# Kernel tuning notes

Measured on AMD Instinct MI355X. Metric: run time of the kernel, lower is better.

The kernel has to match this reference:

```python
import math
import jax, jax.numpy as jnp
import numpy as np

B, S, IN_DIM = 8, 1024, 3
D, H, FF, L, OUT = 512, 8, 2048, 4, 6
DH = D // H


def layernorm(x, g, b, eps=1e-5):
    mu = jnp.mean(x, axis=-1, keepdims=True)
    var = jnp.mean((x - mu) ** 2, axis=-1, keepdims=True)
    return (x - mu) * jax.lax.rsqrt(var + eps) * g + b


def positional_encoding(seq_len, d):
    pos = jnp.arange(seq_len, dtype=jnp.float32)[:, None]
    div = jnp.exp(jnp.arange(0, d, 2, dtype=jnp.float32) * (-math.log(10000.0) / d))
    pe = jnp.zeros((seq_len, d), dtype=jnp.float32)
    pe = pe.at[:, 0::2].set(jnp.sin(pos * div))
    pe = pe.at[:, 1::2].set(jnp.cos(pos * div))
    return pe  # [S, D]


def setup_inputs() -> dict:
    key = jax.random.key(0)
    ks = jax.random.split(key, 16)
    s = 0.02
    inp = {
        'x': jax.random.normal(ks[0], (B, S, IN_DIM), dtype=jnp.float32),
        'Wproj': jax.random.normal(ks[1], (IN_DIM, D), dtype=jnp.float32) * s,
        'bproj': jnp.zeros((D,), jnp.float32),
        'gp': jnp.ones((D,), jnp.float32), 'bp': jnp.zeros((D,), jnp.float32),
        'Wq': jax.random.normal(ks[2], (L, D, D), dtype=jnp.float32) * s,
        'Wk': jax.random.normal(ks[3], (L, D, D), dtype=jnp.float32) * s,
        'Wv': jax.random.normal(ks[4], (L, D, D), dtype=jnp.float32) * s,
        'Wo': jax.random.normal(ks[5], (L, D, D), dtype=jnp.float32) * s,
        'g1': jnp.ones((L, D), jnp.float32), 'b1': jnp.zeros((L, D), jnp.float32),
        'W1': jax.random.normal(ks[6], (L, D, FF), dtype=jnp.float32) * s,
        'W2': jax.random.normal(ks[7], (L, FF, D), dtype=jnp.float32) * s,
        'g2': jnp.ones((L, D), jnp.float32), 'b2': jnp.zeros((L, D), jnp.float32),
        'gf': jnp.ones((D,), jnp.float32), 'bf': jnp.zeros((D,), jnp.float32),
        'Wout': jax.random.normal(ks[8], (D, OUT), dtype=jnp.float32) * s,
        'bout': jnp.zeros((OUT,), jnp.float32),
    }
    return inp


def reference(x, Wproj, bproj, gp, bp, Wq, Wk, Wv, Wo, g1, b1,
              W1, W2, g2, b2, gf, bf, Wout, bout):
    # padding mask: True where all features are zero
    mask = jnp.sum(jnp.abs(x), axis=-1) == 0  # [B, S]
    h = x @ Wproj + bproj                     # [B, S, D]
    h = h + positional_encoding(h.shape[1], D)[None]
    h = layernorm(h, gp, bp)
    scale = 1.0 / math.sqrt(DH)
    for l in range(L):
        q = (h @ Wq[l]).reshape(B, S, H, DH)
        k = (h @ Wk[l]).reshape(B, S, H, DH)
        v = (h @ Wv[l]).reshape(B, S, H, DH)
        scores = jnp.einsum('bqhd,bkhd->bhqk', q, k) * scale  # [B,H,S,S]
        scores = jnp.where(mask[:, None, None, :], -jnp.inf, scores)
        attn = jax.nn.softmax(scores, axis=-1)
        o = jnp.einsum('bhqk,bkhd->bqhd', attn, v).reshape(B, S, D) @ Wo[l]
        h = layernorm(h + o, g1[l], b1[l])
        ff = jax.nn.silu(h @ W1[l]) @ W2[l]
        h = layernorm(h + ff, g2[l], b2[l])
    h = layernorm(h, gf, bf)
    not_pad = (~mask).astype(h.dtype)                      # [B, S]
    pooled = jnp.sum(h * not_pad[..., None], axis=1) / (
        jnp.sum(not_pad, axis=1, keepdims=True) + 1e-8)    # [B, D]
    return pooled @ Wout + bout                            # [B, OUT]
```

## Files before the change

### kernel.cpp

```cpp
#include <hip/hip_runtime.h>
#include <math.h>
#include <stdint.h>

namespace {

constexpr int Bc = 8, Sc = 1024, Dc = 512, Hc = 8, FFc = 2048, Lc = 4, OUTc = 6;
constexpr int QS = 1536;

typedef __attribute__((ext_vector_type(8))) short  bf16x8;
typedef __attribute__((ext_vector_type(4))) float  f32x4;

__device__ __forceinline__ void ld4(float d[4], const float* s) {
    float4 t = *(const float4*)s;
    d[0] = t.x; d[1] = t.y; d[2] = t.z; d[3] = t.w;
}
__device__ __forceinline__ float bf2f(unsigned short u) {
    union { uint32_t i; float f; } c; c.i = ((uint32_t)u) << 16; return c.f;
}
__device__ __forceinline__ unsigned short f2bf(float f) {
    union { float f; uint32_t i; } c; c.f = f;
    uint32_t r = c.i + 0x7FFF + ((c.i >> 16) & 1);
    return (unsigned short)(r >> 16);
}

#define GLDS16(gp, lp) __builtin_amdgcn_global_load_lds(                      \
    (const __attribute__((address_space(1))) uint32_t*)(gp),                  \
    (__attribute__((address_space(3))) uint32_t*)(lp), 16, 0, 0)

__global__ __launch_bounds__(256) void castT(
    const float* __restrict__ in, unsigned short* __restrict__ out,
    int K, int N, size_t in_ls, size_t out_ls)
{
    __shared__ float t[64][65];
    const int k0 = blockIdx.x << 6, n0 = blockIdx.y << 6;
    in  += (size_t)blockIdx.z * in_ls;
    out += (size_t)blockIdx.z * out_ls;
    const int c = threadIdx.x & 63, r4 = threadIdx.x >> 6;
    #pragma unroll
    for (int it = 0; it < 16; ++it) {
        const int r = (it << 2) + r4;
        t[r][c] = in[(size_t)(k0 + r) * N + n0 + c];
    }
    __syncthreads();
    #pragma unroll
    for (int it = 0; it < 16; ++it) {
        const int r = (it << 2) + r4;
        out[(size_t)(n0 + r) * K + k0 + c] = f2bf(t[c][r]);
    }
}

__global__ __launch_bounds__(256) void proj_pe_ln(
    const float* __restrict__ x, const float* __restrict__ Wproj,
    const float* __restrict__ bproj, const float* __restrict__ gp,
    const float* __restrict__ bp, float* __restrict__ h,
    unsigned short* __restrict__ hbf, float* __restrict__ notpad,
    float* __restrict__ maskadd)
{
    const int wave = threadIdx.x >> 6, lane = threadIdx.x & 63;
    const int tok = (blockIdx.x << 2) + wave;
    const int s = tok & (Sc - 1);
    const float x0 = x[tok * 3 + 0], x1 = x[tok * 3 + 1], x2 = x[tok * 3 + 2];
    if (lane == 0) {
        const bool pad = (fabsf(x0) + fabsf(x1) + fabsf(x2) == 0.0f);
        notpad[tok]  = pad ? 0.0f : 1.0f;
        maskadd[tok] = pad ? -1e30f : 0.0f;
    }
    const float c = -logf(10000.0f) / (float)Dc;
    float v[8];
    float sum = 0.f, sumsq = 0.f;
    #pragma unroll
    for (int g = 0; g < 2; ++g) {
        const int dbase = (g << 8) + (lane << 2);
        #pragma unroll
        for (int j = 0; j < 4; ++j) {
            const int d = dbase + j;
            float val = fmaf(x0, Wproj[d],
                        fmaf(x1, Wproj[Dc + d],
                        fmaf(x2, Wproj[2 * Dc + d], bproj[d])));
            const float arg = (float)s * expf((float)(d & ~1) * c);
            val += (d & 1) ? cosf(arg) : sinf(arg);
            v[(g << 2) + j] = val;
            sum += val; sumsq += val * val;
        }
    }
    #pragma unroll
    for (int m = 1; m < 64; m <<= 1) {
        sum   += __shfl_xor(sum, m, 64);
        sumsq += __shfl_xor(sumsq, m, 64);
    }
    const float mu = sum * (1.0f / Dc);
    const float var = sumsq * (1.0f / Dc) - mu * mu;
    const float rstd = rsqrtf(var + 1e-5f);
    #pragma unroll
    for (int g = 0; g < 2; ++g) {
        const int dbase = (g << 8) + (lane << 2);
        float gg[4], bb[4];
        ld4(gg, gp + dbase); ld4(bb, bp + dbase);
        float4 r;
        r.x = (v[(g<<2)+0] - mu) * rstd * gg[0] + bb[0];
        r.y = (v[(g<<2)+1] - mu) * rstd * gg[1] + bb[1];
        r.z = (v[(g<<2)+2] - mu) * rstd * gg[2] + bb[2];
        r.w = (v[(g<<2)+3] - mu) * rstd * gg[3] + bb[3];
        *(float4*)(h + (size_t)tok * Dc + dbase) = r;
        ushort4 rb;
        rb.x = f2bf(r.x); rb.y = f2bf(r.y); rb.z = f2bf(r.z); rb.w = f2bf(r.w);
        *(ushort4*)(hbf + (size_t)tok * Dc + dbase) = rb;
    }
}

__global__ __launch_bounds__(256) void add_ln(
    const float* __restrict__ hin, const unsigned short* __restrict__ delta,
    const float* __restrict__ g, const float* __restrict__ b,
    float* __restrict__ hout, unsigned short* __restrict__ hbf)
{
    const int wave = threadIdx.x >> 6, lane = threadIdx.x & 63;
    const int tok = (blockIdx.x << 2) + wave;
    const float* hp = hin + (size_t)tok * Dc;
    float v[8];
    float sum = 0.f, sumsq = 0.f;
    #pragma unroll
    for (int gI = 0; gI < 2; ++gI) {
        const int dbase = (gI << 8) + (lane << 2);
        float a[4];
        ld4(a, hp + dbase);
        if (delta) {
            ushort4 d4 = *(const ushort4*)(delta + (size_t)tok * Dc + dbase);
            a[0] += bf2f(d4.x); a[1] += bf2f(d4.y);
            a[2] += bf2f(d4.z); a[3] += bf2f(d4.w);
        }
        #pragma unroll
        for (int j = 0; j < 4; ++j) {
            v[(gI << 2) + j] = a[j];
            sum += a[j]; sumsq += a[j] * a[j];
        }
    }
    #pragma unroll
    for (int m = 1; m < 64; m <<= 1) {
        sum   += __shfl_xor(sum, m, 64);
        sumsq += __shfl_xor(sumsq, m, 64);
    }
    const float mu = sum * (1.0f / Dc);
    const float var = sumsq * (1.0f / Dc) - mu * mu;
    const float rstd = rsqrtf(var + 1e-5f);
    #pragma unroll
    for (int gI = 0; gI < 2; ++gI) {
        const int dbase = (gI << 8) + (lane << 2);
        float gg[4], bb[4];
        ld4(gg, g + dbase); ld4(bb, b + dbase);
        float4 r;
        r.x = (v[(gI<<2)+0] - mu) * rstd * gg[0] + bb[0];
        r.y = (v[(gI<<2)+1] - mu) * rstd * gg[1] + bb[1];
        r.z = (v[(gI<<2)+2] - mu) * rstd * gg[2] + bb[2];
        r.w = (v[(gI<<2)+3] - mu) * rstd * gg[3] + bb[3];
        *(float4*)(hout + (size_t)tok * Dc + dbase) = r;
        if (hbf) {
            ushort4 rb;
            rb.x = f2bf(r.x); rb.y = f2bf(r.y); rb.z = f2bf(r.z); rb.w = f2bf(r.w);
            *(ushort4*)(hbf + (size_t)tok * Dc + dbase) = rb;
        }
    }
}

template<int EPI, int NT>
__global__ __launch_bounds__(256) void gemm_bf16(
    const unsigned short* __restrict__ A, const unsigned short* __restrict__ Bt,
    void* __restrict__ Cv, void* __restrict__ Cv2, int M, int N, int K)
{
    constexpr int JN = NT / 32;
    __shared__ unsigned short As[128 * 32];
    __shared__ unsigned short Bs[NT * 32];
    __shared__ unsigned short Tr[(EPI == 3) ? 128 * 128 : 1];
    const int tid = threadIdx.x;
    const int wave = tid >> 6, lane = tid & 63;
    const int m0 = blockIdx.y << 7;
    const int n0 = blockIdx.x * NT;
    const int wm = (wave >> 1) << 6;
    const int wn = (wave & 1) * (NT / 2);
    const int lrow = lane >> 2;
    const int lcol = (lane & 3) << 3;
    const int l15 = lane & 15;
    const int lg = lane >> 4;
    const int krow = lg << 3;

    f32x4 acc[4][JN] = {};

    for (int k0 = 0; k0 < K; k0 += 32) {
        __syncthreads();
        #pragma unroll
        for (int t = 0; t < 2; ++t) {
            const int rbase = (t << 6) + (wave << 4);
            GLDS16(A + (size_t)(m0 + rbase + lrow) * K + k0 + lcol, &As[rbase * 32]);
        }
        #pragma unroll
        for (int t = 0; t < NT / 64; ++t) {
            const int rbase = (t << 6) + (wave << 4);
            GLDS16(Bt + (size_t)(n0 + rbase + lrow) * K + k0 + lcol, &Bs[rbase * 32]);
        }
        __syncthreads();
        bf16x8 af[4], bfr[JN];
        #pragma unroll
        for (int i = 0; i < 4; ++i)
            af[i] = *(const bf16x8*)&As[(wm + (i << 4) + l15) * 32 + krow];
        #pragma unroll
        for (int j = 0; j < JN; ++j)
            bfr[j] = *(const bf16x8*)&Bs[(wn + (j << 4) + l15) * 32 + krow];
        #pragma unroll
        for (int i = 0; i < 4; ++i)
            #pragma unroll
            for (int j = 0; j < JN; ++j)
                acc[i][j] = __builtin_amdgcn_mfma_f32_16x16x32_bf16(
                    af[i], bfr[j], acc[i][j], 0, 0, 0);
    }

    if constexpr (EPI == 3) {
        if (n0 >= 1024) {
            __syncthreads();
            #pragma unroll
            for (int i = 0; i < 4; ++i)
                #pragma unroll
                for (int j = 0; j < JN; ++j)
                    #pragma unroll
                    for (int r = 0; r < 4; ++r) {
                        const int lm = wm + (i << 4) + (lg << 2) + r;
                        const int ln = wn + (j << 4) + l15;
                        Tr[ln * 128 + lm] = f2bf(acc[i][j][r]);
                    }
            __syncthreads();
            const int bb = m0 >> 10, s0 = m0 & 1023;
            #pragma unroll
            for (int it = 0; it < 8; ++it) {
                const int idx = (it << 8) + tid;
                const int ln = idx >> 4, lmc = (idx & 15) << 3;
                const int gcol = n0 - 1024 + ln;
                const int head = gcol >> 6, dh = gcol & 63;
                *(bf16x8*)((unsigned short*)Cv2 +
                    (size_t)((((bb << 3) + head) << 6) + dh) * 1024 + s0 + lmc) =
                    *(const bf16x8*)&Tr[ln * 128 + lmc];
            }
            return;
        }
    }

    const int crow0 = m0 + wm + (lg << 2);
    const int ccol0 = n0 + wn + l15;
    #pragma unroll
    for (int i = 0; i < 4; ++i)
        #pragma unroll
        for (int j = 0; j < JN; ++j)
            #pragma unroll
            for (int r = 0; r < 4; ++r) {
                const int row = crow0 + (i << 4) + r;
                const int col = ccol0 + (j << 4);
                float v = acc[i][j][r];
                if (EPI == 3) {
                    if (n0 < 512) v *= 0.125f;
                    ((unsigned short*)Cv)[(size_t)row * 1024 + col] = f2bf(v);
                } else {
                    if (EPI == 1) v = v / (1.0f + expf(-v));
                    ((unsigned short*)Cv)[(size_t)row * N + col] = f2bf(v);
                }
            }
}

__global__ __launch_bounds__(256) void attn_mfma(
    const unsigned short* __restrict__ qk,
    const unsigned short* __restrict__ vT,
    const float* __restrict__ maskadd,
    unsigned short* __restrict__ o)
{
    __shared__ unsigned short Ks[2][128][32];
    __shared__ unsigned short Vs[4][64][32];
    __shared__ unsigned short Ps[4][16][132];
    __shared__ float Madd[128];
    const int tid = threadIdx.x;
    const int wave = tid >> 6, lane = tid & 63;
    const int qt = blockIdx.x & 15;
    const int hh = (blockIdx.x >> 4) & 7;
    const int b  = blockIdx.x >> 7;
    const int q0 = qt << 6;
    const int l15 = lane & 15, lg = lane >> 4;
    const int srow = lane >> 2;
    const int scol = (lane & 3) << 3;

    #pragma unroll
    for (int p = 0; p < 2; ++p)
        GLDS16(qk + (size_t)((b << 10) + q0 + (wave << 4) + srow) * 1024
                  + (hh << 6) + (p << 5) + scol,
               &Ks[p][wave << 4][0]);
    __syncthreads();
    bf16x8 qf[2];
    qf[0] = *(const bf16x8*)&Ks[0][(wave << 4) + l15][lg << 3];
    qf[1] = *(const bf16x8*)&Ks[1][(wave << 4) + l15][lg << 3];

    f32x4 oacc[4] = {};
    float l_part[4] = {0.f, 0.f, 0.f, 0.f};

    for (int kt = 0; kt < 8; ++kt) {
        const int k0 = kt << 7;
        __syncthreads();
        #pragma unroll
        for (int t = 0; t < 2; ++t) {
            const int rbase = (t << 6) + (wave << 4);
            #pragma unroll
            for (int p = 0; p < 2; ++p)
                GLDS16(qk + (size_t)((b << 10) + k0 + rbase + srow) * 1024
                          + 512 + (hh << 6) + (p << 5) + scol,
                       &Ks[p][rbase][0]);
        }
        #pragma unroll
        for (int p = 0; p < 4; ++p)
            GLDS16(vT + (size_t)(((b << 3) + hh) * 64 + (wave << 4) + srow) * 1024
                      + k0 + (p << 5) + scol,
                   &Vs[p][wave << 4][0]);
        if (tid < 128) Madd[tid] = maskadd[(b << 10) + k0 + tid];
        __syncthreads();

        f32x4 sacc[8];
        #pragma unroll
        for (int j = 0; j < 8; ++j) {
            sacc[j] = (f32x4){0.f, 0.f, 0.f, 0.f};
            #pragma unroll
            for (int p = 0; p < 2; ++p) {
                const bf16x8 kf = *(const bf16x8*)&Ks[p][(j << 4) + l15][lg << 3];
                sacc[j] = __builtin_amdgcn_mfma_f32_16x16x32_bf16(qf[p], kf, sacc[j], 0, 0, 0);
            }
        }

        #pragma unroll
        for (int j = 0; j < 8; ++j) {
            const float ma = Madd[(j << 4) + l15];
            #pragma unroll
            for (int r = 0; r < 4; ++r) {
                const float p = __expf(sacc[j][r] + ma);
                l_part[r] += p;
                Ps[wave][(lg << 2) + r][(j << 4) + l15] = f2bf(p);
            }
        }
        __asm__ volatile("s_waitcnt lgkmcnt(0)" ::: "memory");

        #pragma unroll
        for (int kp = 0; kp < 4; ++kp) {
            const bf16x8 pa = *(const bf16x8*)&Ps[wave][l15][(kp << 5) + (lg << 3)];
            #pragma unroll
            for (int j = 0; j < 4; ++j) {
                const bf16x8 vf = *(const bf16x8*)&Vs[kp][(j << 4) + l15][lg << 3];
                oacc[j] = __builtin_amdgcn_mfma_f32_16x16x32_bf16(pa, vf, oacc[j], 0, 0, 0);
            }
        }
    }

    #pragma unroll
    for (int r = 0; r < 4; ++r) {
        float l = l_part[r];
        #pragma unroll
        for (int m = 1; m < 16; m <<= 1) l += __shfl_xor(l, m, 64);
        l_part[r] = 1.0f / l;
    }
    const int tokr = (b << 10) + q0 + (wave << 4) + (lg << 2);
    #pragma unroll
    for (int j = 0; j < 4; ++j)
        #pragma unroll
        for (int r = 0; r < 4; ++r)
            o[(size_t)(tokr + r) * 512 + (hh << 6) + (j << 4) + l15] =
                f2bf(oacc[j][r] * l_part[r]);
}

__global__ __launch_bounds__(256) void pool_kernel(
    const float* __restrict__ h, const float* __restrict__ notpad,
    float* __restrict__ pooled, float* __restrict__ counts)
{
    const int b = blockIdx.y;
    const int s0 = blockIdx.x << 5;
    const int t = threadIdx.x;
    float a0 = 0.f, a1 = 0.f;
    for (int ss = 0; ss < 32; ++ss) {
        const float w = notpad[(b << 10) + s0 + ss];
        const float* hp = h + (size_t)((b << 10) + s0 + ss) * Dc;
        a0 = fmaf(w, hp[t], a0);
        a1 = fmaf(w, hp[t + 256], a1);
    }
    atomicAdd(&pooled[b * Dc + t], a0);
    atomicAdd(&pooled[b * Dc + t + 256], a1);
    if (t < 32) {
        float w = notpad[(b << 10) + s0 + t];
        #pragma unroll
        for (int m = 1; m < 32; m <<= 1) w += __shfl_xor(w, m, 64);
        if (t == 0) atomicAdd(&counts[b], w);
    }
}

__global__ void out_kernel(
    const float* __restrict__ pooled, const float* __restrict__ counts,
    const float* __restrict__ Wout, const float* __restrict__ bout,
    float* __restrict__ out)
{
    const int bo = blockIdx.x;
    const int b = bo / OUTc, oc = bo % OUTc;
    const int lane = threadIdx.x;
    float acc = 0.f;
    for (int d = lane; d < Dc; d += 64)
        acc = fmaf(pooled[b * Dc + d], Wout[(size_t)d * OUTc + oc], acc);
    #pragma unroll
    for (int m = 1; m < 64; m <<= 1) acc += __shfl_xor(acc, m, 64);
    if (lane == 0) out[b * OUTc + oc] = acc / (counts[b] + 1e-8f) + bout[oc];
}

}

extern "C" void kernel_launch(void* const* d_in, const int* in_sizes, int n_in,
                              void* d_out, int out_size, void* d_ws, size_t ws_size,
                              hipStream_t stream)
{
    (void)in_sizes; (void)n_in; (void)out_size; (void)ws_size;
    const float* x     = (const float*)d_in[0];
    const float* Wproj = (const float*)d_in[1];
    const float* bproj = (const float*)d_in[2];
    const float* gp    = (const float*)d_in[3];
    const float* bp    = (const float*)d_in[4];
    const float* Wq    = (const float*)d_in[5];
    const float* Wk    = (const float*)d_in[6];
    const float* Wv    = (const float*)d_in[7];
    const float* Wo    = (const float*)d_in[8];
    const float* g1    = (const float*)d_in[9];
    const float* b1    = (const float*)d_in[10];
    const float* W1    = (const float*)d_in[11];
    const float* W2    = (const float*)d_in[12];
    const float* g2    = (const float*)d_in[13];
    const float* b2    = (const float*)d_in[14];
    const float* gf    = (const float*)d_in[15];
    const float* bf    = (const float*)d_in[16];
    const float* Wout  = (const float*)d_in[17];
    const float* bout  = (const float*)d_in[18];
    float* out = (float*)d_out;

    const size_t MiB = 1u << 20;
    char* base = (char*)d_ws;
    float*          h       = (float*)(base);
    unsigned short* h_bf    = (unsigned short*)(base + 16 * MiB);
    unsigned short* qk_act  = (unsigned short*)(base + 24 * MiB);
    unsigned short* vT      = (unsigned short*)(base + 40 * MiB);
    unsigned short* ob_bf   = (unsigned short*)(base + 48 * MiB);
    unsigned short* bufB_bf = (unsigned short*)(base + 56 * MiB);
    unsigned short* ffa_bf  = (unsigned short*)(base + 24 * MiB);
    unsigned short* qkvT    = (unsigned short*)(base + 72 * MiB);
    unsigned short* WoT     = (unsigned short*)(base + 78 * MiB);
    unsigned short* W1T     = (unsigned short*)(base + 80 * MiB);
    unsigned short* W2T     = (unsigned short*)(base + 88 * MiB);
    float*          notpad  = (float*)(base + 96 * MiB);
    float*          maskadd = notpad + 8192;
    float*          pooled  = maskadd + 8192;
    float*          counts  = pooled + Bc * Dc;

    const int M = Bc * Sc;

    castT<<<dim3(8, 8, Lc), 256, 0, stream>>>(Wq, qkvT,               512, 512, (size_t)512*512, (size_t)QS*512);
    castT<<<dim3(8, 8, Lc), 256, 0, stream>>>(Wk, qkvT + 512 * 512,   512, 512, (size_t)512*512, (size_t)QS*512);
    castT<<<dim3(8, 8, Lc), 256, 0, stream>>>(Wv, qkvT + 1024 * 512,  512, 512, (size_t)512*512, (size_t)QS*512);
    castT<<<dim3(8, 8, Lc), 256, 0, stream>>>(Wo, WoT,                512, 512, (size_t)512*512, (size_t)512*512);
    castT<<<dim3(8, 32, Lc), 256, 0, stream>>>(W1, W1T, 512, 2048, (size_t)512*2048, (size_t)2048*512);
    castT<<<dim3(32, 8, Lc), 256, 0, stream>>>(W2, W2T, 2048, 512, (size_t)2048*512, (size_t)512*2048);

    proj_pe_ln<<<M / 4, 256, 0, stream>>>(x, Wproj, bproj, gp, bp, h, h_bf, notpad, maskadd);

    for (int l = 0; l < Lc; ++l) {
        gemm_bf16<3, 128><<<dim3(QS / 128, M / 128), 256, 0, stream>>>(
            h_bf, qkvT + (size_t)l * QS * 512, qk_act, vT, M, QS, 512);
        attn_mfma<<<Bc * Hc * (Sc / 64), 256, 0, stream>>>(qk_act, vT, maskadd, ob_bf);
        gemm_bf16<2, 64><<<dim3(512 / 64, M / 128), 256, 0, stream>>>(
            ob_bf, WoT + (size_t)l * 512 * 512, bufB_bf, nullptr, M, 512, 512);
        add_ln<<<M / 4, 256, 0, stream>>>(h, bufB_bf, g1 + (size_t)l * Dc, b1 + (size_t)l * Dc, h, h_bf);
        gemm_bf16<1, 128><<<dim3(FFc / 128, M / 128), 256, 0, stream>>>(
            h_bf, W1T + (size_t)l * FFc * 512, ffa_bf, nullptr, M, FFc, 512);
        gemm_bf16<2, 64><<<dim3(512 / 64, M / 128), 256, 0, stream>>>(
            ffa_bf, W2T + (size_t)l * 512 * FFc, bufB_bf, nullptr, M, 512, FFc);
        add_ln<<<M / 4, 256, 0, stream>>>(h, bufB_bf, g2 + (size_t)l * Dc, b2 + (size_t)l * Dc, h, h_bf);
    }
    add_ln<<<M / 4, 256, 0, stream>>>(h, nullptr, gf, bf, h, nullptr);

    hipMemsetAsync(pooled, 0, (size_t)(Bc * Dc + Bc) * sizeof(float), stream);
    pool_kernel<<<dim3(Sc / 32, Bc), 256, 0, stream>>>(h, notpad, pooled, counts);
    out_kernel<<<Bc * OUTc, 64, 0, stream>>>(pooled, counts, Wout, bout, out);
}
```

Measured before the change: 901.2 us.

## Fuse weight casts, deepen GEMM K-tile with swizzled LDS, enlarge attention query tile

Six weight-transpose/cast launches become one castAll kernel. The bf16 GEMM now stages a 64-wide K slice per iteration with an XOR-swizzled LDS layout to avoid bank conflicts and halve the barrier count. The transpose scratch buffer reuses the A/B LDS with a padded stride. Attention blocks now handle 128 queries each (two 16-row sub-tiles per wave), so K/V tiles are reused across twice as many queries, at the cost of more registers, with launch_bounds hinting 2 blocks per SIMD.

```diff
diff --git a/kernel.cpp b/kernel.cpp
--- a/kernel.cpp
+++ b/kernel.cpp
@@ -27,25 +27,48 @@
     (const __attribute__((address_space(1))) uint32_t*)(gp),                  \
     (__attribute__((address_space(3))) uint32_t*)(lp), 16, 0, 0)
 
-__global__ __launch_bounds__(256) void castT(
-    const float* __restrict__ in, unsigned short* __restrict__ out,
-    int K, int N, size_t in_ls, size_t out_ls)
-{
-    __shared__ float t[64][65];
-    const int k0 = blockIdx.x << 6, n0 = blockIdx.y << 6;
-    in  += (size_t)blockIdx.z * in_ls;
-    out += (size_t)blockIdx.z * out_ls;
+__global__ __launch_bounds__(256) void castAll(
+    const float* __restrict__ Wq, const float* __restrict__ Wk,
+    const float* __restrict__ Wv, const float* __restrict__ Wo,
+    const float* __restrict__ W1, const float* __restrict__ W2,
+    unsigned short* __restrict__ qkvT, unsigned short* __restrict__ WoT,
+    unsigned short* __restrict__ W1T, unsigned short* __restrict__ W2T)
+{
+    const int t = blockIdx.x;
+    const float* in; unsigned short* out; int K, N, k0, n0;
+    if (t < 1024) {
+        const int mat = t >> 6, l = mat >> 2, w = mat & 3;
+        K = 512; N = 512;
+        k0 = ((t >> 3) & 7) << 6; n0 = (t & 7) << 6;
+        const float* ws4[4] = {Wq, Wk, Wv, Wo};
+        in = ws4[w] + (size_t)l * 512 * 512;
+        out = (w < 3) ? qkvT + (size_t)l * QS * 512 + (size_t)w * 512 * 512
+                      : WoT + (size_t)l * 512 * 512;
+    } else if (t < 2048) {
+        const int u = t - 1024, l = u >> 8;
+        K = 512; N = 2048;
+        k0 = ((u >> 5) & 7) << 6; n0 = (u & 31) << 6;
+        in = W1 + (size_t)l * 512 * 2048;
+        out = W1T + (size_t)l * 2048 * 512;
+    } else {
+        const int u = t - 2048, l = u >> 8;
+        K = 2048; N = 512;
+        k0 = ((u >> 3) & 31) << 6; n0 = (u & 7) << 6;
+        in = W2 + (size_t)l * 2048 * 512;
+        out = W2T + (size_t)l * 512 * 2048;
+    }
+    __shared__ float tbuf[64][65];
     const int c = threadIdx.x & 63, r4 = threadIdx.x >> 6;
     #pragma unroll
     for (int it = 0; it < 16; ++it) {
         const int r = (it << 2) + r4;
-        t[r][c] = in[(size_t)(k0 + r) * N + n0 + c];
+        tbuf[r][c] = in[(size_t)(k0 + r) * N + n0 + c];
     }
     __syncthreads();
     #pragma unroll
     for (int it = 0; it < 16; ++it) {
         const int r = (it << 2) + r4;
-        out[(size_t)(n0 + r) * K + k0 + c] = f2bf(t[c][r]);
+        out[(size_t)(n0 + r) * K + k0 + c] = f2bf(tbuf[c][r]);
     }
 }
 
@@ -167,64 +190,69 @@
     void* __restrict__ Cv, void* __restrict__ Cv2, int M, int N, int K)
 {
     constexpr int JN = NT / 32;
-    __shared__ unsigned short As[128 * 32];
-    __shared__ unsigned short Bs[NT * 32];
-    __shared__ unsigned short Tr[(EPI == 3) ? 128 * 128 : 1];
+    constexpr int ABsz = 128 * 64 + NT * 64;
+    constexpr int TRst = 136;
+    constexpr int SMsz = (EPI == 3 && 128 * TRst > ABsz) ? 128 * TRst : ABsz;
+    __shared__ unsigned short smem[SMsz];
+    unsigned short* As = smem;
+    unsigned short* Bs = smem + 128 * 64;
     const int tid = threadIdx.x;
     const int wave = tid >> 6, lane = tid & 63;
     const int m0 = blockIdx.y << 7;
     const int n0 = blockIdx.x * NT;
     const int wm = (wave >> 1) << 6;
     const int wn = (wave & 1) * (NT / 2);
-    const int lrow = lane >> 2;
-    const int lcol = (lane & 3) << 3;
     const int l15 = lane & 15;
-    const int lg = lane >> 4;
-    const int krow = lg << 3;
+    const int lg  = lane >> 4;
+    const int grow  = lane >> 3;
+    const int gcolk = ((lane & 7) ^ grow) << 3;
 
     f32x4 acc[4][JN] = {};
 
-    for (int k0 = 0; k0 < K; k0 += 32) {
+    for (int k0 = 0; k0 < K; k0 += 64) {
         __syncthreads();
         #pragma unroll
-        for (int t = 0; t < 2; ++t) {
-            const int rbase = (t << 6) + (wave << 4);
-            GLDS16(A + (size_t)(m0 + rbase + lrow) * K + k0 + lcol, &As[rbase * 32]);
-        }
-        #pragma unroll
-        for (int t = 0; t < NT / 64; ++t) {
-            const int rbase = (t << 6) + (wave << 4);
-            GLDS16(Bt + (size_t)(n0 + rbase + lrow) * K + k0 + lcol, &Bs[rbase * 32]);
+        for (int t = 0; t < 4; ++t) {
+            const int rb = (t << 5) + (wave << 3);
+            GLDS16(A + (size_t)(m0 + rb + grow) * K + k0 + gcolk, &As[rb * 64]);
+        }
+        #pragma unroll
+        for (int t = 0; t < NT / 32; ++t) {
+            const int rb = (t << 5) + (wave << 3);
+            GLDS16(Bt + (size_t)(n0 + rb + grow) * K + k0 + gcolk, &Bs[rb * 64]);
         }
         __syncthreads();
-        bf16x8 af[4], bfr[JN];
-        #pragma unroll
-        for (int i = 0; i < 4; ++i)
-            af[i] = *(const bf16x8*)&As[(wm + (i << 4) + l15) * 32 + krow];
-        #pragma unroll
-        for (int j = 0; j < JN; ++j)
-            bfr[j] = *(const bf16x8*)&Bs[(wn + (j << 4) + l15) * 32 + krow];
-        #pragma unroll
-        for (int i = 0; i < 4; ++i)
+        #pragma unroll
+        for (int h = 0; h < 2; ++h) {
+            const int sw = (((h << 2) + lg) ^ (l15 & 7)) << 3;
+            bf16x8 af[4], bfr[JN];
+            #pragma unroll
+            for (int i = 0; i < 4; ++i)
+                af[i] = *(const bf16x8*)&As[(wm + (i << 4) + l15) * 64 + sw];
             #pragma unroll
             for (int j = 0; j < JN; ++j)
-                acc[i][j] = __builtin_amdgcn_mfma_f32_16x16x32_bf16(
-                    af[i], bfr[j], acc[i][j], 0, 0, 0);
+                bfr[j] = *(const bf16x8*)&Bs[(wn + (j << 4) + l15) * 64 + sw];
+            #pragma unroll
+            for (int i = 0; i < 4; ++i)
+                #pragma unroll
+                for (int j = 0; j < JN; ++j)
+                    acc[i][j] = __builtin_amdgcn_mfma_f32_16x16x32_bf16(
+                        af[i], bfr[j], acc[i][j], 0, 0, 0);
+        }
     }
 
     if constexpr (EPI == 3) {
         if (n0 >= 1024) {
             __syncthreads();
+            unsigned short* Tr = smem;
             #pragma unroll
             for (int i = 0; i < 4; ++i)
                 #pragma unroll
                 for (int j = 0; j < JN; ++j)
                     #pragma unroll
-                    for (int r = 0; r < 4; ++r) {
-                        const int lm = wm + (i << 4) + (lg << 2) + r;
-                        const int ln = wn + (j << 4) + l15;
-                        Tr[ln * 128 + lm] = f2bf(acc[i][j][r]);
-                    }
+                    for (int r = 0; r < 4; ++r)
+                        Tr[(wn + (j << 4) + l15) * TRst + wm + (i << 4) + (lg << 2) + r]
+                            = f2bf(acc[i][j][r]);
             __syncthreads();
             const int bb = m0 >> 10, s0 = m0 & 1023;
             #pragma unroll
@@ -235,7 +263,7 @@
                 const int head = gcol >> 6, dh = gcol & 63;
                 *(bf16x8*)((unsigned short*)Cv2 +
                     (size_t)((((bb << 3) + head) << 6) + dh) * 1024 + s0 + lmc) =
-                    *(const bf16x8*)&Tr[ln * 128 + lmc];
+                    *(const bf16x8*)&Tr[ln * TRst + lmc];
             }
             return;
         }
@@ -262,107 +290,124 @@
             }
 }
 
-__global__ __launch_bounds__(256) void attn_mfma(
+__global__ __launch_bounds__(256, 2) void attn_mfma(
     const unsigned short* __restrict__ qk,
     const unsigned short* __restrict__ vT,
     const float* __restrict__ maskadd,
     unsigned short* __restrict__ o)
 {
+    constexpr int PST = 124;
     __shared__ unsigned short Ks[2][128][32];
     __shared__ unsigned short Vs[4][64][32];
-    __shared__ unsigned short Ps[4][16][132];
+    __shared__ unsigned short Ps[4][32][PST];
     __shared__ float Madd[128];
     const int tid = threadIdx.x;
     const int wave = tid >> 6, lane = tid & 63;
-    const int qt = blockIdx.x & 15;
-    const int hh = (blockIdx.x >> 4) & 7;
-    const int b  = blockIdx.x >> 7;
-    const int q0 = qt << 6;
+    const int b  = blockIdx.x & 7;
+    const int hh = (blockIdx.x >> 3) & 7;
+    const int qt = blockIdx.x >> 6;
+    const int q0 = qt << 7;
     const int l15 = lane & 15, lg = lane >> 4;
     const int srow = lane >> 2;
     const int scol = (lane & 3) << 3;
 
     #pragma unroll
-    for (int p = 0; p < 2; ++p)
-        GLDS16(qk + (size_t)((b << 10) + q0 + (wave << 4) + srow) * 1024
-                  + (hh << 6) + (p << 5) + scol,
-               &Ks[p][wave << 4][0]);
+    for (int t = 0; t < 2; ++t)
+        #pragma unroll
+        for (int p = 0; p < 2; ++p)
+            GLDS16(qk + (size_t)((b << 10) + q0 + (t << 6) + (wave << 4) + srow) * 1024
+                      + (hh << 6) + (p << 5) + scol,
+                   &Ks[p][(t << 6) + (wave << 4)][0]);
     __syncthreads();
-    bf16x8 qf[2];
-    qf[0] = *(const bf16x8*)&Ks[0][(wave << 4) + l15][lg << 3];
-    qf[1] = *(const bf16x8*)&Ks[1][(wave << 4) + l15][lg << 3];
-
-    f32x4 oacc[4] = {};
-    float l_part[4] = {0.f, 0.f, 0.f, 0.f};
+    bf16x8 qf[2][2];
+    #pragma unroll
+    for (int s = 0; s < 2; ++s)
+        #pragma unroll
+        for (int p = 0; p < 2; ++p)
+            qf[s][p] = *(const bf16x8*)&Ks[p][(s << 6) + (wave << 4) + l15][lg << 3];
+
+    f32x4 oacc[2][4] = {};
+    float l_part[2][4] = {};
 
     for (int kt = 0; kt < 8; ++kt) {
         const int k0 = kt << 7;
         __syncthreads();
         #pragma unroll
-        for (int t = 0; t < 2; ++t) {
-            const int rbase = (t << 6) + (wave << 4);
+        for (int t = 0; t < 2; ++t)
             #pragma unroll
             for (int p = 0; p < 2; ++p)
-                GLDS16(qk + (size_t)((b << 10) + k0 + rbase + srow) * 1024
+                GLDS16(qk + (size_t)((b << 10) + k0 + (t << 6) + (wave << 4) + srow) * 1024
                           + 512 + (hh << 6) + (p << 5) + scol,
-                       &Ks[p][rbase][0]);
-        }
-        #pragma unroll
-        for (int p = 0; p < 4; ++p)
-            GLDS16(vT + (size_t)(((b << 3) + hh) * 64 + (wave << 4) + srow) * 1024
-                      + k0 + (p << 5) + scol,
-                   &Vs[p][wave << 4][0]);
+                       &Ks[p][(t << 6) + (wave << 4)][0]);
+        #pragma unroll
+        for (int kp = 0; kp < 4; ++kp)
+            GLDS16(vT + (size_t)((((b << 3) + hh) << 6) + (wave << 4) + srow) * 1024
+                      + k0 + (kp << 5) + scol,
+                   &Vs[kp][wave << 4][0]);
         if (tid < 128) Madd[tid] = maskadd[(b << 10) + k0 + tid];
         __syncthreads();
 
-        f32x4 sacc[8];
+        f32x4 sacc[2][8] = {};
         #pragma unroll
         for (int j = 0; j < 8; ++j) {
-            sacc[j] = (f32x4){0.f, 0.f, 0.f, 0.f};
-            #pragma unroll
-            for (int p = 0; p < 2; ++p) {
-                const bf16x8 kf = *(const bf16x8*)&Ks[p][(j << 4) + l15][lg << 3];
-                sacc[j] = __builtin_amdgcn_mfma_f32_16x16x32_bf16(qf[p], kf, sacc[j], 0, 0, 0);
+            const bf16x8 kf0 = *(const bf16x8*)&Ks[0][(j << 4) + l15][lg << 3];
+            const bf16x8 kf1 = *(const bf16x8*)&Ks[1][(j << 4) + l15][lg << 3];
+            #pragma unroll
+            for (int s = 0; s < 2; ++s) {
+                sacc[s][j] = __builtin_amdgcn_mfma_f32_16x16x32_bf16(qf[s][0], kf0, sacc[s][j], 0, 0, 0);
+                sacc[s][j] = __builtin_amdgcn_mfma_f32_16x16x32_bf16(qf[s][1], kf1, sacc[s][j], 0, 0, 0);
             }
         }
 
         #pragma unroll
-        for (int j = 0; j < 8; ++j) {
-            const float ma = Madd[(j << 4) + l15];
-            #pragma unroll
-            for (int r = 0; r < 4; ++r) {
-                const float p = __expf(sacc[j][r] + ma);
-                l_part[r] += p;
-                Ps[wave][(lg << 2) + r][(j << 4) + l15] = f2bf(p);
+        for (int s = 0; s < 2; ++s)
+            #pragma unroll
+            for (int j = 0; j < 8; ++j) {
+                const float ma = Madd[(j << 4) + l15];
+                #pragma unroll
+                for (int r = 0; r < 4; ++r) {
+                    const float p = __expf(sacc[s][j][r] + ma);
+                    l_part[s][r] += p;
+                    Ps[wave][(s << 4) + (lg << 2) + r][(j << 4) + l15] = f2bf(p);
+                }
             }
-        }
         __asm__ volatile("s_waitcnt lgkmcnt(0)" ::: "memory");
 
         #pragma unroll
         for (int kp = 0; kp < 4; ++kp) {
-            const bf16x8 pa = *(const bf16x8*)&Ps[wave][l15][(kp << 5) + (lg << 3)];
-            #pragma unroll
-            for (int j = 0; j < 4; ++j) {
-                const bf16x8 vf = *(const bf16x8*)&Vs[kp][(j << 4) + l15][lg << 3];
-                oacc[j] = __builtin_amdgcn_mfma_f32_16x16x32_bf16(pa, vf, oacc[j], 0, 0, 0);
+            bf16x8 vf[4];
+            #pragma unroll
+            for (int j = 0; j < 4; ++j)
+                vf[j] = *(const bf16x8*)&Vs[kp][(j << 4) + l15][lg << 3];
+            #pragma unroll
+            for (int s = 0; s < 2; ++s) {
+                const bf16x8 pa = *(const bf16x8*)&Ps[wave][(s << 4) + l15][(kp << 5) + (lg << 3)];
+                #pragma unroll
+                for (int j = 0; j < 4; ++j)
+                    oacc[s][j] = __builtin_amdgcn_mfma_f32_16x16x32_bf16(pa, vf[j], oacc[s][j], 0, 0, 0);
             }
         }
     }
 
     #pragma unroll
-    for (int r = 0; r < 4; ++r) {
-        float l = l_part[r];
-        #pragma unroll
-        for (int m = 1; m < 16; m <<= 1) l += __shfl_xor(l, m, 64);
-        l_part[r] = 1.0f / l;
-    }
-    const int tokr = (b << 10) + q0 + (wave << 4) + (lg << 2);
-    #pragma unroll
-    for (int j = 0; j < 4; ++j)
-        #pragma unroll
-        for (int r = 0; r < 4; ++r)
-            o[(size_t)(tokr + r) * 512 + (hh << 6) + (j << 4) + l15] =
-                f2bf(oacc[j][r] * l_part[r]);
+    for (int s = 0; s < 2; ++s)
+        #pragma unroll
+        for (int r = 0; r < 4; ++r) {
+            float l = l_part[s][r];
+            #pragma unroll
+            for (int m = 1; m < 16; m <<= 1) l += __shfl_xor(l, m, 64);
+            l_part[s][r] = 1.0f / l;
+        }
+    #pragma unroll
+    for (int s = 0; s < 2; ++s) {
+        const int tokr = (b << 10) + q0 + (s << 6) + (wave << 4) + (lg << 2);
+        #pragma unroll
+        for (int j = 0; j < 4; ++j)
+            #pragma unroll
+            for (int r = 0; r < 4; ++r)
+                o[(size_t)(tokr + r) * 512 + (hh << 6) + (j << 4) + l15] =
+                    f2bf(oacc[s][j][r] * l_part[s][r]);
+    }
 }
 
 __global__ __launch_bounds__(256) void pool_kernel(
@@ -453,19 +498,13 @@
 
     const int M = Bc * Sc;
 
-    castT<<<dim3(8, 8, Lc), 256, 0, stream>>>(Wq, qkvT,               512, 512, (size_t)512*512, (size_t)QS*512);
-    castT<<<dim3(8, 8, Lc), 256, 0, stream>>>(Wk, qkvT + 512 * 512,   512, 512, (size_t)512*512, (size_t)QS*512);
-    castT<<<dim3(8, 8, Lc), 256, 0, stream>>>(Wv, qkvT + 1024 * 512,  512, 512, (size_t)512*512, (size_t)QS*512);
-    castT<<<dim3(8, 8, Lc), 256, 0, stream>>>(Wo, WoT,                512, 512, (size_t)512*512, (size_t)512*512);
-    castT<<<dim3(8, 32, Lc), 256, 0, stream>>>(W1, W1T, 512, 2048, (size_t)512*2048, (size_t)2048*512);
-    castT<<<dim3(32, 8, Lc), 256, 0, stream>>>(W2, W2T, 2048, 512, (size_t)2048*512, (size_t)512*2048);
-
+    castAll<<<3072, 256, 0, stream>>>(Wq, Wk, Wv, Wo, W1, W2, qkvT, WoT, W1T, W2T);
     proj_pe_ln<<<M / 4, 256, 0, stream>>>(x, Wproj, bproj, gp, bp, h, h_bf, notpad, maskadd);
 
     for (int l = 0; l < Lc; ++l) {
         gemm_bf16<3, 128><<<dim3(QS / 128, M / 128), 256, 0, stream>>>(
             h_bf, qkvT + (size_t)l * QS * 512, qk_act, vT, M, QS, 512);
-        attn_mfma<<<Bc * Hc * (Sc / 64), 256, 0, stream>>>(qk_act, vT, maskadd, ob_bf);
+        attn_mfma<<<Bc * Hc * (Sc / 128), 256, 0, stream>>>(qk_act, vT, maskadd, ob_bf);
         gemm_bf16<2, 64><<<dim3(512 / 64, M / 128), 256, 0, stream>>>(
             ob_bf, WoT + (size_t)l * 512 * 512, bufB_bf, nullptr, M, 512, 512);
         add_ln<<<M / 4, 256, 0, stream>>>(h, bufB_bf, g1 + (size_t)l * Dc, b1 + (size_t)l * Dc, h, h_bf);
```

New measurement: 816.2 us. -9.4%, faster.
